# Performance work log

Measured on AMD Instinct MI355X. Metric: run time of the kernel, lower is better.

The kernel has to match this reference:

```python
import jax, jax.numpy as jnp
import numpy as np
import math

H = 16          # n_heads
D = 1024        # hidden_dim
HD = D // H     # head_dim = 64
LR = 256        # Linformer low-rank length L
MAX_T = 4096    # max_seq_len


def setup_inputs() -> dict:
    key = jax.random.key(0)
    ks = jax.random.split(key, 7)
    X = jax.random.normal(ks[0], (4, 4096, D), dtype=jnp.float32)
    # lecun_normal ~ N(0, 1/fan_in)
    W_kernel = jax.random.normal(ks[1], (D, 3 * D), dtype=jnp.float32) / math.sqrt(D)
    W_bias = jnp.zeros((3 * D,), dtype=jnp.float32)
    low_rank_E = jax.random.normal(ks[2], (MAX_T, H, LR), dtype=jnp.float32) / math.sqrt(MAX_T)
    low_rank_V = jax.random.normal(ks[3], (MAX_T, H, LR), dtype=jnp.float32) / math.sqrt(MAX_T)
    o_kernel = jax.random.normal(ks[4], (D, D), dtype=jnp.float32) / math.sqrt(D)
    o_bias = jnp.zeros((D,), dtype=jnp.float32)
    return {"X": X, "W_kernel": W_kernel, "W_bias": W_bias,
            "low_rank_E": low_rank_E, "low_rank_V": low_rank_V,
            "o_kernel": o_kernel, "o_bias": o_bias}


def reference(X, W_kernel, W_bias, low_rank_E, low_rank_V, o_kernel, o_bias):
    B, T, _ = X.shape
    # L2-normalize tokens
    norm = jnp.linalg.norm(X, ord=2, axis=-1, keepdims=True)  # (B,T,1)
    Xn = X / norm
    # fused QKV projection
    qkv = Xn @ W_kernel + W_bias                 # (B,T,3D)
    qkv = qkv.reshape(B, T, 3, H, HD)
    Q, K, V = qkv[:, :, 0], qkv[:, :, 1], qkv[:, :, 2]   # (B,T,H,HD)
    # low-rank sequence projection of K/V: T -> L
    E = low_rank_E[:T]                            # (T,H,L)
    F = low_rank_V[:T]                            # (T,H,L)
    Kp = jnp.einsum('THK,BTHD->BHKD', E, K)       # (B,H,L,HD)
    Vp = jnp.einsum('THK,BTHD->BHKD', F, V)       # (B,H,L,HD)
    Qh = Q.transpose(0, 2, 1, 3)                  # (B,H,T,HD)
    logits = jnp.einsum('BHTD,BHKD->BHTK', Qh, Kp) / math.sqrt(HD)
    attn = jax.nn.softmax(logits, axis=-1)        # (B,H,T,L)
    out = jnp.einsum('BHTK,BHKD->BHTD', attn, Vp) # (B,H,T,HD)
    out = out.transpose(0, 2, 1, 3).reshape(B, T, H * HD)
    return out @ o_kernel + o_bias
```

## Files before the change

### kernel.cpp

```cpp
#include <hip/hip_runtime.h>
#include <stdint.h>

typedef unsigned short u16;
typedef uint32_t u32;
typedef __bf16 bf16x8 __attribute__((ext_vector_type(8)));
typedef float f32x4 __attribute__((ext_vector_type(4)));

__device__ __forceinline__ u16 f2bf(float f) {
    u32 u = __builtin_bit_cast(u32, f);
    u += 0x7fffu + ((u >> 16) & 1u);
    return (u16)(u >> 16);
}

__device__ __forceinline__ f32x4 mfma16(bf16x8 a, bf16x8 b, f32x4 c) {
    return __builtin_amdgcn_mfma_f32_16x16x32_bf16(a, b, c, 0, 0, 0);
}

__device__ __forceinline__ void gld_lds16(void* lds, const void* g) {
    __builtin_amdgcn_global_load_lds(
        (__attribute__((address_space(1))) void*)(uintptr_t)g,
        (__attribute__((address_space(3))) void*)(u32)(uintptr_t)lds,
        16, 0, 0);
}

__global__ __launch_bounds__(256) void k_norm(const float* __restrict__ X,
                                              u16* __restrict__ Xn) {
    const int row = blockIdx.x;
    const float4 v = ((const float4*)(X + (size_t)row * 1024))[threadIdx.x];
    float ss = v.x * v.x + v.y * v.y + v.z * v.z + v.w * v.w;
#pragma unroll
    for (int m = 1; m < 64; m <<= 1) ss += __shfl_xor(ss, m);
    __shared__ float red[4];
    if ((threadIdx.x & 63) == 0) red[threadIdx.x >> 6] = ss;
    __syncthreads();
    const float sc = 1.0f / sqrtf(red[0] + red[1] + red[2] + red[3]);
    ushort4 o;
    o.x = f2bf(v.x * sc); o.y = f2bf(v.y * sc);
    o.z = f2bf(v.z * sc); o.w = f2bf(v.w * sc);
    ((ushort4*)(Xn + (size_t)row * 1024))[threadIdx.x] = o;
}

__global__ __launch_bounds__(256) void k_transpose_cast64(
    const float* __restrict__ src, u16* __restrict__ dst,
    int R, int rstride, long zsrc, long zdst) {
    __shared__ float tile[64][65];
    src += (size_t)blockIdx.z * zsrc;
    dst += (size_t)blockIdx.z * zdst;
    const int c0 = blockIdx.x * 64, r0 = blockIdx.y * 64;
    const int tid = threadIdx.x;
    const int lr = tid >> 4, lc = tid & 15;
#pragma unroll
    for (int i = 0; i < 4; ++i) {
        const int r = lr + i * 16;
        const float4 v = *(const float4*)(src + (size_t)(r0 + r) * rstride + c0 + lc * 4);
        tile[r][lc * 4 + 0] = v.x; tile[r][lc * 4 + 1] = v.y;
        tile[r][lc * 4 + 2] = v.z; tile[r][lc * 4 + 3] = v.w;
    }
    __syncthreads();
    const int c = tid >> 2, seg = tid & 3;
    u32 w[8];
#pragma unroll
    for (int j = 0; j < 8; ++j) {
        const u32 lo = f2bf(tile[seg * 16 + 2 * j][c]);
        const u32 hi = f2bf(tile[seg * 16 + 2 * j + 1][c]);
        w[j] = lo | (hi << 16);
    }
    u16* dp = dst + (size_t)(c0 + c) * R + r0 + seg * 16;
    uint4 q0; q0.x = w[0]; q0.y = w[1]; q0.z = w[2]; q0.w = w[3];
    uint4 q1; q1.x = w[4]; q1.y = w[5]; q1.z = w[6]; q1.w = w[7];
    *(uint4*)dp = q0;
    *((uint4*)dp + 1) = q1;
}

#define G256_PRE(Aptr, Bptr, LDA_, LDB_)                                          \
    const int tid = threadIdx.x, lane = tid & 63, wid = tid >> 6;                 \
    const int wm = wid >> 2, wn = wid & 3;                                        \
    const int cl = lane & 15, g = lane >> 4;                                      \
    const int srow = tid >> 2;                                                    \
    const int scol = ((tid & 3) ^ ((tid >> 3) & 3)) * 8;                          \
    const u16* pA0 = (Aptr) + (size_t)(m0 + srow) * (LDA_) + scol;                \
    const u16* pA1 = pA0 + (size_t)128 * (LDA_);                                  \
    const u16* pB0 = (Bptr) + (size_t)(n0 + srow) * (LDB_) + scol;                \
    const u16* pB1 = pB0 + (size_t)128 * (LDB_);                                  \
    u32 offA[8], offB[4];                                                         \
    _Pragma("unroll")                                                             \
    for (int mf = 0; mf < 8; ++mf) {                                              \
        const int r = wm * 128 + mf * 16 + cl;                                    \
        offA[mf] = r * 64 + ((g ^ ((r >> 1) & 3)) * 16);                          \
    }                                                                             \
    _Pragma("unroll")                                                             \
    for (int nf = 0; nf < 4; ++nf) {                                              \
        const int r = wn * 64 + nf * 16 + cl;                                     \
        offB[nf] = 65536 + r * 64 + ((g ^ ((r >> 1) & 3)) * 16);                  \
    }

#define G256_STAGE(kt)                                                            \
    {                                                                             \
        const u32 bo = ((kt) & 3) * 16384;                                        \
        gld_lds16(sm + bo + tid * 16,                 pA0 + (kt) * 32);           \
        gld_lds16(sm + bo + 8192 + tid * 16,          pA1 + (kt) * 32);           \
        gld_lds16(sm + 65536 + bo + tid * 16,         pB0 + (kt) * 32);           \
        gld_lds16(sm + 65536 + bo + 8192 + tid * 16,  pB1 + (kt) * 32);           \
    }

#define G256_LOOP(NKT)                                                            \
    G256_STAGE(0) G256_STAGE(1) G256_STAGE(2)                                     \
    for (int kt = 0; kt < (NKT); ++kt) {                                          \
        if (kt < (NKT) - 3) {                                                     \
            G256_STAGE(kt + 3)                                                    \
            asm volatile("s_waitcnt vmcnt(12)" ::: "memory");                     \
        } else if (kt == (NKT) - 3) {                                             \
            asm volatile("s_waitcnt vmcnt(8)" ::: "memory");                      \
        } else if (kt == (NKT) - 2) {                                             \
            asm volatile("s_waitcnt vmcnt(4)" ::: "memory");                      \
        } else {                                                                  \
            asm volatile("s_waitcnt vmcnt(0)" ::: "memory");                      \
        }                                                                         \
        __builtin_amdgcn_s_barrier();                                             \
        const char* bk = sm + (kt & 3) * 16384;                                   \
        bf16x8 aF[4], bF[4];                                                      \
        _Pragma("unroll")                                                         \
        for (int mf = 0; mf < 4; ++mf) aF[mf] = *(const bf16x8*)(bk + offA[mf]);  \
        _Pragma("unroll")                                                         \
        for (int nf = 0; nf < 4; ++nf) bF[nf] = *(const bf16x8*)(bk + offB[nf]);  \
        asm volatile("s_waitcnt lgkmcnt(0)" ::: "memory");                        \
        __builtin_amdgcn_sched_barrier(0);                                        \
        __builtin_amdgcn_s_setprio(1);                                            \
        _Pragma("unroll")                                                         \
        for (int mf = 0; mf < 4; ++mf)                                            \
            _Pragma("unroll")                                                     \
            for (int nf = 0; nf < 4; ++nf)                                        \
                acc[mf][nf] = mfma16(aF[mf], bF[nf], acc[mf][nf]);                \
        __builtin_amdgcn_s_setprio(0);                                            \
        bf16x8 aG[4];                                                             \
        _Pragma("unroll")                                                         \
        for (int mf = 0; mf < 4; ++mf) aG[mf] = *(const bf16x8*)(bk + offA[mf + 4]); \
        asm volatile("s_waitcnt lgkmcnt(0)" ::: "memory");                        \
        __builtin_amdgcn_sched_barrier(0);                                        \
        __builtin_amdgcn_s_setprio(1);                                            \
        _Pragma("unroll")                                                         \
        for (int mf = 0; mf < 4; ++mf)                                            \
            _Pragma("unroll")                                                     \
            for (int nf = 0; nf < 4; ++nf)                                        \
                acc[mf + 4][nf] = mfma16(aG[mf], bF[nf], acc[mf + 4][nf]);        \
        __builtin_amdgcn_s_setprio(0);                                            \
        __builtin_amdgcn_s_barrier();                                             \
    }

__global__ __launch_bounds__(512, 2) void k_gemm_qkv(
    const u16* __restrict__ A, const u16* __restrict__ Bt,
    const float* __restrict__ bias,
    u16* __restrict__ Qo, u16* __restrict__ Kt, u16* __restrict__ Vt) {
    __shared__ __align__(16) char sm[131072];
    u32 bid = blockIdx.x;
    bid = (bid & 7) * 96 + (bid >> 3);
    const int m0 = (int)(bid / 12) * 256, n0 = (int)(bid % 12) * 256;

    G256_PRE(A, Bt, 1024, 1024)

    const f32x4 fz = {0.f, 0.f, 0.f, 0.f};
    f32x4 acc[8][4];
#pragma unroll
    for (int i = 0; i < 8; ++i)
#pragma unroll
        for (int j = 0; j < 4; ++j) acc[i][j] = fz;

    G256_LOOP(32)

#pragma unroll
    for (int mf = 0; mf < 8; ++mf) {
        const int mbase = m0 + wm * 128 + mf * 16 + g * 4;
        const int b = mbase >> 12;
        const int t = mbase & 4095;
#pragma unroll
        for (int nf = 0; nf < 4; ++nf) {
            const int n = n0 + wn * 64 + nf * 16 + cl;
            const float bv = bias[n];
            const int seg = n >> 10;
            const int hd = n & 1023;
            f32x4 v = acc[mf][nf];
            if (seg == 0) {
#pragma unroll
                for (int r = 0; r < 4; ++r)
                    Qo[(size_t)(mbase + r) * 1024 + hd] = f2bf(v[r] + bv);
            } else {
                u16* dst = (seg == 1) ? Kt : Vt;
                ushort4 pk;
                pk.x = f2bf(v[0] + bv); pk.y = f2bf(v[1] + bv);
                pk.z = f2bf(v[2] + bv); pk.w = f2bf(v[3] + bv);
                *(ushort4*)(dst + (size_t)(b * 1024 + hd) * 4096 + t) = pk;
            }
        }
    }
}

__global__ __launch_bounds__(512, 2) void k_gemm_out(
    const u16* __restrict__ A, const u16* __restrict__ Bt,
    const float* __restrict__ bias, float* __restrict__ out) {
    __shared__ __align__(16) char sm[131072];
    u32 bid = blockIdx.x;
    bid = (bid & 7) * 32 + (bid >> 3);
    const int m0 = (int)(bid / 4) * 256, n0 = (int)(bid % 4) * 256;

    G256_PRE(A, Bt, 1024, 1024)

    const f32x4 fz = {0.f, 0.f, 0.f, 0.f};
    f32x4 acc[8][4];
#pragma unroll
    for (int i = 0; i < 8; ++i)
#pragma unroll
        for (int j = 0; j < 4; ++j) acc[i][j] = fz;

    G256_LOOP(32)

#pragma unroll
    for (int mf = 0; mf < 8; ++mf) {
        const int mbase = m0 + wm * 128 + mf * 16 + g * 4;
#pragma unroll
        for (int nf = 0; nf < 4; ++nf) {
            const int n = n0 + wn * 64 + nf * 16 + cl;
            const float bv = bias[n];
            f32x4 v = acc[mf][nf];
#pragma unroll
            for (int r = 0; r < 4; ++r)
                out[(size_t)(mbase + r) * 1024 + n] = v[r] + bv;
        }
    }
}

__global__ __launch_bounds__(256) void k_gemm_kpvp(
    const u16* __restrict__ Et, const u16* __restrict__ Ft,
    const u16* __restrict__ Kt, const u16* __restrict__ Vt,
    u16* __restrict__ Kp, u16* __restrict__ Vpt) {
    __shared__ __align__(16) char sm[24576];
    const int tid = threadIdx.x, lane = tid & 63, wid = tid >> 6;
    const int wm = wid >> 1, wn = wid & 1;
    const int cl = lane & 15, g = lane >> 4;
    const int mT = blockIdx.x;
    const int bh = blockIdx.y;
    const int h = bh & 15;
    const int s = blockIdx.z;

    const u16* Abase = (s == 0 ? Et : Ft) + (size_t)h * (256 * 4096);
    const u16* Bbase = (s == 0 ? Kt : Vt) + (size_t)bh * (64 * 4096);
    const u16* gA0 = Abase + (size_t)(mT * 128 + (tid >> 2)) * 4096 + (tid & 3) * 8;
    const u16* gA1 = gA0 + (size_t)64 * 4096;
    const u16* gB0 = Bbase + (size_t)(tid >> 2) * 4096 + (tid & 3) * 8;

    const f32x4 fz = {0.f, 0.f, 0.f, 0.f};
    f32x4 acc[4][2];
#pragma unroll
    for (int i = 0; i < 4; ++i) { acc[i][0] = fz; acc[i][1] = fz; }

    gld_lds16(sm + tid * 16, gA0); gld_lds16(sm + 4096 + tid * 16, gA1);
    gld_lds16(sm + 8192 + tid * 16, gB0);
    gA0 += 32; gA1 += 32; gB0 += 32;

    u32 roff = 0;
    for (int k0 = 0; k0 < 4096; k0 += 32) {
        const u32 woff = roff ^ 12288;
        if (k0 + 32 < 4096) {
            gld_lds16(sm + woff + tid * 16, gA0); gld_lds16(sm + woff + 4096 + tid * 16, gA1);
            gld_lds16(sm + woff + 8192 + tid * 16, gB0);
            gA0 += 32; gA1 += 32; gB0 += 32;
            asm volatile("s_waitcnt vmcnt(3)" ::: "memory");
        } else {
            asm volatile("s_waitcnt vmcnt(0)" ::: "memory");
        }
        __builtin_amdgcn_s_barrier();
        __builtin_amdgcn_sched_barrier(0);
        const char* rb = sm + roff;
        bf16x8 aF[4], bF[2];
#pragma unroll
        for (int mf = 0; mf < 4; ++mf)
            aF[mf] = *(const bf16x8*)(rb + (wm * 64 + mf * 16 + cl) * 64 + g * 16);
#pragma unroll
        for (int nf = 0; nf < 2; ++nf)
            bF[nf] = *(const bf16x8*)(rb + 8192 + (wn * 32 + nf * 16 + cl) * 64 + g * 16);
#pragma unroll
        for (int mf = 0; mf < 4; ++mf)
#pragma unroll
            for (int nf = 0; nf < 2; ++nf)
                acc[mf][nf] = mfma16(aF[mf], bF[nf], acc[mf][nf]);
        asm volatile("s_waitcnt lgkmcnt(0)" ::: "memory");
        __builtin_amdgcn_s_barrier();
        roff = woff;
    }

    const size_t obase = (size_t)bh * 16384;
#pragma unroll
    for (int mf = 0; mf < 4; ++mf) {
        const int m = mT * 128 + wm * 64 + mf * 16 + g * 4;
#pragma unroll
        for (int nf = 0; nf < 2; ++nf) {
            const int n = wn * 32 + nf * 16 + cl;
            f32x4 v = acc[mf][nf];
            if (s == 0) {
#pragma unroll
                for (int r = 0; r < 4; ++r)
                    Kp[obase + (size_t)(m + r) * 64 + n] = f2bf(v[r]);
            } else {
                ushort4 pk;
                pk.x = f2bf(v[0]); pk.y = f2bf(v[1]);
                pk.z = f2bf(v[2]); pk.w = f2bf(v[3]);
                *(ushort4*)(Vpt + obase + (size_t)n * 256 + m) = pk;
            }
        }
    }
}

__global__ __launch_bounds__(256, 1) void k_attn(
    const u16* __restrict__ Q, const u16* __restrict__ Kp,
    const u16* __restrict__ Vpt, u16* __restrict__ AO) {
    __shared__ __align__(16) char sm[65536];
    const int lane = threadIdx.x & 63, wid = threadIdx.x >> 6;
    const int cl = lane & 15, g = lane >> 4;
    const int tT = blockIdx.x, h = blockIdx.y, b = blockIdx.z;
    const int bh = b * 16 + h;
    const int trow0 = b * 4096 + tT * 128 + wid * 32;
    const u16* Qb = Q + (size_t)trow0 * 1024 + h * 64;
    const u16* KpB = Kp + (size_t)bh * (256 * 64);
    const u16* VpB = Vpt + (size_t)bh * (64 * 256);
    char* sP = sm + wid * 16384;

    bf16x8 qF[2][2];
#pragma unroll
    for (int nf = 0; nf < 2; ++nf)
#pragma unroll
        for (int ks = 0; ks < 2; ++ks)
            qF[nf][ks] = *(const bf16x8*)(Qb + (size_t)(nf * 16 + cl) * 1024 + ks * 32 + g * 8);

    const f32x4 fz = {0.f, 0.f, 0.f, 0.f};
    f32x4 Sp[16][2];
#pragma unroll
    for (int mf = 0; mf < 16; ++mf) { Sp[mf][0] = fz; Sp[mf][1] = fz; }

#pragma unroll
    for (int mf = 0; mf < 16; ++mf) {
#pragma unroll
        for (int ks = 0; ks < 2; ++ks) {
            bf16x8 aF = *(const bf16x8*)(KpB + (size_t)(mf * 16 + cl) * 64 + ks * 32 + g * 8);
            Sp[mf][0] = mfma16(aF, qF[0][ks], Sp[mf][0]);
            Sp[mf][1] = mfma16(aF, qF[1][ks], Sp[mf][1]);
        }
    }

    float inv_sum[2];
#pragma unroll
    for (int nf = 0; nf < 2; ++nf) {
        float mx = -1e30f;
#pragma unroll
        for (int mf = 0; mf < 16; ++mf)
#pragma unroll
            for (int r = 0; r < 4; ++r) {
                float x = Sp[mf][nf][r] * 0.125f;
                Sp[mf][nf][r] = x;
                mx = fmaxf(mx, x);
            }
        mx = fmaxf(mx, __shfl_xor(mx, 16));
        mx = fmaxf(mx, __shfl_xor(mx, 32));
        float sum = 0.f;
#pragma unroll
        for (int mf = 0; mf < 16; ++mf)
#pragma unroll
            for (int r = 0; r < 4; ++r) {
                float p = __expf(Sp[mf][nf][r] - mx);
                Sp[mf][nf][r] = p;
                sum += p;
            }
        sum += __shfl_xor(sum, 16);
        sum += __shfl_xor(sum, 32);
        inv_sum[nf] = 1.0f / sum;

        const int tl = nf * 16 + cl;
        const int sw = (tl & 7) << 4;
#pragma unroll
        for (int mf = 0; mf < 16; ++mf) {
            uint2 pk;
            pk.x = (u32)f2bf(Sp[mf][nf][0]) | ((u32)f2bf(Sp[mf][nf][1]) << 16);
            pk.y = (u32)f2bf(Sp[mf][nf][2]) | ((u32)f2bf(Sp[mf][nf][3]) << 16);
            *(uint2*)(sP + ((tl * 512 + (mf * 16 + g * 4) * 2) ^ sw)) = pk;
        }
    }

    f32x4 Oa[4][2];
#pragma unroll
    for (int mf = 0; mf < 4; ++mf) { Oa[mf][0] = fz; Oa[mf][1] = fz; }
#pragma unroll
    for (int ks = 0; ks < 8; ++ks) {
        bf16x8 aF[4];
#pragma unroll
        for (int mf = 0; mf < 4; ++mf)
            aF[mf] = *(const bf16x8*)(VpB + (size_t)(mf * 16 + cl) * 256 + ks * 32 + g * 8);
#pragma unroll
        for (int nf = 0; nf < 2; ++nf) {
            const int tl = nf * 16 + cl;
            const int sw = (tl & 7) << 4;
            bf16x8 bF = *(const bf16x8*)(sP + ((tl * 512 + (ks * 32 + g * 8) * 2) ^ sw));
#pragma unroll
            for (int mf = 0; mf < 4; ++mf)
                Oa[mf][nf] = mfma16(aF[mf], bF, Oa[mf][nf]);
        }
    }

#pragma unroll
    for (int nf = 0; nf < 2; ++nf) {
        const int t = trow0 + nf * 16 + cl;
#pragma unroll
        for (int mf = 0; mf < 4; ++mf) {
            f32x4 v = Oa[mf][nf];
            ushort4 pk;
            pk.x = f2bf(v[0] * inv_sum[nf]); pk.y = f2bf(v[1] * inv_sum[nf]);
            pk.z = f2bf(v[2] * inv_sum[nf]); pk.w = f2bf(v[3] * inv_sum[nf]);
            *(ushort4*)(AO + (size_t)t * 1024 + h * 64 + mf * 16 + g * 4) = pk;
        }
    }
}

extern "C" void kernel_launch(void* const* d_in, const int* in_sizes, int n_in,
                              void* d_out, int out_size, void* d_ws, size_t ws_size,
                              hipStream_t stream) {
    const float* X  = (const float*)d_in[0];
    const float* Wk = (const float*)d_in[1];
    const float* Wb = (const float*)d_in[2];
    const float* E  = (const float*)d_in[3];
    const float* F  = (const float*)d_in[4];
    const float* Ok = (const float*)d_in[5];
    const float* Ob = (const float*)d_in[6];
    float* out = (float*)d_out;
    char* ws = (char*)d_ws;

    u16* Xn  = (u16*)(ws + 0);
    u16* Wt  = (u16*)(ws + 33554432);
    u16* Ot  = (u16*)(ws + 39845888);
    u16* Et  = (u16*)(ws + 41943040);
    u16* Ft  = (u16*)(ws + 75497472);
    u16* Qb  = (u16*)(ws + 109051904);
    u16* Kt  = (u16*)(ws + 142606336);
    u16* Vt  = (u16*)(ws + 176160768);
    u16* Kp  = (u16*)(ws + 209715200);
    u16* Vpt = (u16*)(ws + 211812352);
    u16* AO  = Xn;

    k_norm<<<16384, 256, 0, stream>>>(X, Xn);
    k_transpose_cast64<<<dim3(48, 16, 1), 256, 0, stream>>>(Wk, Wt, 1024, 3072, 0, 0);
    k_transpose_cast64<<<dim3(16, 16, 1), 256, 0, stream>>>(Ok, Ot, 1024, 1024, 0, 0);
    k_transpose_cast64<<<dim3(4, 64, 16), 256, 0, stream>>>(E, Et, 4096, 4096, 256, 1048576);
    k_transpose_cast64<<<dim3(4, 64, 16), 256, 0, stream>>>(F, Ft, 4096, 4096, 256, 1048576);
    k_gemm_qkv<<<768, 512, 0, stream>>>(Xn, Wt, Wb, Qb, Kt, Vt);
    k_gemm_kpvp<<<dim3(2, 64, 2), 256, 0, stream>>>(Et, Ft, Kt, Vt, Kp, Vpt);
    k_attn<<<dim3(32, 16, 4), 256, 0, stream>>>(Qb, Kp, Vpt, AO);
    k_gemm_out<<<256, 512, 0, stream>>>(AO, Ot, Ob, out);
}
```

Baseline: 404.5 us.

## Rework 256x256 GEMM main loop to K=64 double-buffered stages with interleaved loads

Replaces the 4-stage K=32 pipeline in the QKV and output projection GEMMs with a 2-buffer K=64 scheme. Each LDS stage is split into four quarter-tiles, and global-to-LDS loads for the next stage are issued between MFMA groups to overlap copy with compute. It also changes the LDS swizzle to a 128-byte row XOR pattern and halves the number of barrier-synchronised iterations. The tradeoff is more barriers per stage, since one follows each quarter MMA block, and reduced prefetch depth.

After: 387.7 us. 1.04x faster.

```diff
diff --git a/kernel.cpp b/kernel.cpp
--- a/kernel.cpp
+++ b/kernel.cpp
@@ -72,79 +72,94 @@
     *((uint4*)dp + 1) = q1;
 }
 
-#define G256_PRE(Aptr, Bptr, LDA_, LDB_)                                          \
-    const int tid = threadIdx.x, lane = tid & 63, wid = tid >> 6;                 \
-    const int wm = wid >> 2, wn = wid & 3;                                        \
-    const int cl = lane & 15, g = lane >> 4;                                      \
-    const int srow = tid >> 2;                                                    \
-    const int scol = ((tid & 3) ^ ((tid >> 3) & 3)) * 8;                          \
-    const u16* pA0 = (Aptr) + (size_t)(m0 + srow) * (LDA_) + scol;                \
-    const u16* pA1 = pA0 + (size_t)128 * (LDA_);                                  \
-    const u16* pB0 = (Bptr) + (size_t)(n0 + srow) * (LDB_) + scol;                \
-    const u16* pB1 = pB0 + (size_t)128 * (LDB_);                                  \
-    u32 offA[8], offB[4];                                                         \
-    _Pragma("unroll")                                                             \
-    for (int mf = 0; mf < 8; ++mf) {                                              \
-        const int r = wm * 128 + mf * 16 + cl;                                    \
-        offA[mf] = r * 64 + ((g ^ ((r >> 1) & 3)) * 16);                          \
-    }                                                                             \
-    _Pragma("unroll")                                                             \
-    for (int nf = 0; nf < 4; ++nf) {                                              \
-        const int r = wn * 64 + nf * 16 + cl;                                     \
-        offB[nf] = 65536 + r * 64 + ((g ^ ((r >> 1) & 3)) * 16);                  \
-    }
-
-#define G256_STAGE(kt)                                                            \
-    {                                                                             \
-        const u32 bo = ((kt) & 3) * 16384;                                        \
-        gld_lds16(sm + bo + tid * 16,                 pA0 + (kt) * 32);           \
-        gld_lds16(sm + bo + 8192 + tid * 16,          pA1 + (kt) * 32);           \
-        gld_lds16(sm + 65536 + bo + tid * 16,         pB0 + (kt) * 32);           \
-        gld_lds16(sm + 65536 + bo + 8192 + tid * 16,  pB1 + (kt) * 32);           \
-    }
-
-#define G256_LOOP(NKT)                                                            \
-    G256_STAGE(0) G256_STAGE(1) G256_STAGE(2)                                     \
-    for (int kt = 0; kt < (NKT); ++kt) {                                          \
-        if (kt < (NKT) - 3) {                                                     \
-            G256_STAGE(kt + 3)                                                    \
-            asm volatile("s_waitcnt vmcnt(12)" ::: "memory");                     \
-        } else if (kt == (NKT) - 3) {                                             \
-            asm volatile("s_waitcnt vmcnt(8)" ::: "memory");                      \
-        } else if (kt == (NKT) - 2) {                                             \
-            asm volatile("s_waitcnt vmcnt(4)" ::: "memory");                      \
-        } else {                                                                  \
-            asm volatile("s_waitcnt vmcnt(0)" ::: "memory");                      \
-        }                                                                         \
-        __builtin_amdgcn_s_barrier();                                             \
-        const char* bk = sm + (kt & 3) * 16384;                                   \
-        bf16x8 aF[4], bF[4];                                                      \
-        _Pragma("unroll")                                                         \
-        for (int mf = 0; mf < 4; ++mf) aF[mf] = *(const bf16x8*)(bk + offA[mf]);  \
-        _Pragma("unroll")                                                         \
-        for (int nf = 0; nf < 4; ++nf) bF[nf] = *(const bf16x8*)(bk + offB[nf]);  \
-        asm volatile("s_waitcnt lgkmcnt(0)" ::: "memory");                        \
-        __builtin_amdgcn_sched_barrier(0);                                        \
-        __builtin_amdgcn_s_setprio(1);                                            \
-        _Pragma("unroll")                                                         \
-        for (int mf = 0; mf < 4; ++mf)                                            \
-            _Pragma("unroll")                                                     \
-            for (int nf = 0; nf < 4; ++nf)                                        \
-                acc[mf][nf] = mfma16(aF[mf], bF[nf], acc[mf][nf]);                \
-        __builtin_amdgcn_s_setprio(0);                                            \
-        bf16x8 aG[4];                                                             \
-        _Pragma("unroll")                                                         \
-        for (int mf = 0; mf < 4; ++mf) aG[mf] = *(const bf16x8*)(bk + offA[mf + 4]); \
-        asm volatile("s_waitcnt lgkmcnt(0)" ::: "memory");                        \
-        __builtin_amdgcn_sched_barrier(0);                                        \
-        __builtin_amdgcn_s_setprio(1);                                            \
-        _Pragma("unroll")                                                         \
-        for (int mf = 0; mf < 4; ++mf)                                            \
-            _Pragma("unroll")                                                     \
-            for (int nf = 0; nf < 4; ++nf)                                        \
-                acc[mf + 4][nf] = mfma16(aG[mf], bF[nf], acc[mf + 4][nf]);        \
-        __builtin_amdgcn_s_setprio(0);                                            \
-        __builtin_amdgcn_s_barrier();                                             \
+#define G8_PRE(Aptr, Bptr)                                                       \
+    const int tid = threadIdx.x, lane = tid & 63;                                \
+    const int wid = tid >> 6, wm = wid >> 2, wn = wid & 3;                       \
+    const int cl = lane & 15, g = lane >> 4;                                     \
+    const int colb = (tid & 7) * 16;                                             \
+    const int scb = colb ^ (((tid >> 3) & 7) << 4);                              \
+    const int rbA = ((tid >> 3) & 31) + ((tid >> 8) << 7);                       \
+    const int rbB = tid >> 3;                                                    \
+    const char* gA = (const char*)(Aptr) + (size_t)(m0 + rbA) * 2048 + scb;      \
+    const char* gB = (const char*)(Bptr) + (size_t)(n0 + rbB) * 2048 + scb;      \
+    const u32 lA = (u32)(rbA * 128 + colb);                                      \
+    const u32 lB = (u32)(65536 + rbB * 128 + colb);                              \
+    const int xr0 = (g * 16) ^ ((cl & 7) << 4);                                  \
+    const int xr1 = (64 + g * 16) ^ ((cl & 7) << 4);
+
+#define G8_STA(q, tau, beta) gld_lds16(sm + (beta) + lA + (q) * 4096,            \
+                                       gA + (q) * 65536 + (size_t)(tau) * 128);
+#define G8_STB(c, tau, beta) gld_lds16(sm + (beta) + lB + (c) * 8192,            \
+                                       gB + (c) * 131072 + (size_t)(tau) * 128);
+
+#define G8_RDB(beta)                                                             \
+    _Pragma("unroll") for (int nf = 0; nf < 4; ++nf) {                           \
+        const u32 rb_ = (beta) + 65536 + (u32)(wn * 64 + nf * 16 + cl) * 128;    \
+        bF[nf][0] = *(const bf16x8*)(sm + rb_ + xr0);                            \
+        bF[nf][1] = *(const bf16x8*)(sm + rb_ + xr1);                            \
+    }
+#define G8_RDA(q, beta)                                                          \
+    _Pragma("unroll") for (int m = 0; m < 2; ++m) {                              \
+        const u32 ra_ = (beta) + (u32)(wm * 128 + (q) * 32 + m * 16 + cl) * 128; \
+        aF[m][0] = *(const bf16x8*)(sm + ra_ + xr0);                             \
+        aF[m][1] = *(const bf16x8*)(sm + ra_ + xr1);                             \
+    }
+
+#define G8_MMA(q)                                                                \
+    asm volatile("s_waitcnt lgkmcnt(0)" ::: "memory");                           \
+    __builtin_amdgcn_sched_barrier(0);                                           \
+    __builtin_amdgcn_s_setprio(1);                                               \
+    _Pragma("unroll") for (int m = 0; m < 2; ++m)                                \
+        _Pragma("unroll") for (int nf = 0; nf < 4; ++nf) {                       \
+            acc[(q)*2 + m][nf] = mfma16(aF[m][0], bF[nf][0], acc[(q)*2 + m][nf]);\
+            acc[(q)*2 + m][nf] = mfma16(aF[m][1], bF[nf][1], acc[(q)*2 + m][nf]);\
+        }                                                                        \
+    __builtin_amdgcn_s_setprio(0);                                               \
+    __builtin_amdgcn_s_barrier();                                                \
+    __builtin_amdgcn_sched_barrier(0);
+
+#define G8_LOOP                                                                  \
+    bf16x8 aF[2][2], bF[4][2];                                                   \
+    G8_STA(0, 0, 0) G8_STB(0, 0, 0) G8_STA(1, 0, 0) G8_STB(1, 0, 0)              \
+    G8_STA(2, 0, 0) G8_STB(2, 0, 0) G8_STA(3, 0, 0) G8_STB(3, 0, 0)              \
+    G8_STA(0, 1, 32768) G8_STB(0, 1, 32768)                                      \
+    G8_STA(1, 1, 32768) G8_STB(1, 1, 32768)                                      \
+    G8_STA(2, 1, 32768) G8_STB(2, 1, 32768)                                      \
+    for (int it = 0; it < 8; ++it) {                                             \
+        const int t1 = 2 * it + 1, t2v = 2 * it + 2, t3v = 2 * it + 3;           \
+        const bool nt = (it < 7);                                                \
+                                                                         \
+        G8_STA(3, t1, 32768) G8_STB(3, t1, 32768)                                \
+        asm volatile("s_waitcnt vmcnt(8)" ::: "memory");                         \
+        __builtin_amdgcn_s_barrier();                                            \
+        G8_RDB(0) G8_RDA(0, 0) G8_MMA(0)                                         \
+                                                                         \
+        if (nt) { G8_STA(0, t2v, 0) G8_STB(0, t2v, 0) }                          \
+        G8_RDA(1, 0) G8_MMA(1)                                                   \
+                                                                         \
+        if (nt) { G8_STA(1, t2v, 0) G8_STB(1, t2v, 0) }                          \
+        G8_RDA(2, 0) G8_MMA(2)                                                   \
+                                                                         \
+        if (nt) { G8_STA(2, t2v, 0) G8_STB(2, t2v, 0) }                          \
+        G8_RDA(3, 0) G8_MMA(3)                                                   \
+                                                                         \
+        if (nt) {                                                                \
+            G8_STA(3, t2v, 0) G8_STB(3, t2v, 0)                                  \
+            asm volatile("s_waitcnt vmcnt(8)" ::: "memory");                     \
+        } else {                                                                 \
+            asm volatile("s_waitcnt vmcnt(0)" ::: "memory");                     \
+        }                                                                        \
+        __builtin_amdgcn_s_barrier();                                            \
+        G8_RDB(32768) G8_RDA(0, 32768) G8_MMA(0)                                 \
+                                                                         \
+        if (nt) { G8_STA(0, t3v, 32768) G8_STB(0, t3v, 32768) }                  \
+        G8_RDA(1, 32768) G8_MMA(1)                                               \
+                                                                         \
+        if (nt) { G8_STA(1, t3v, 32768) G8_STB(1, t3v, 32768) }                  \
+        G8_RDA(2, 32768) G8_MMA(2)                                               \
+                                                                         \
+        if (nt) { G8_STA(2, t3v, 32768) G8_STB(2, t3v, 32768) }                  \
+        G8_RDA(3, 32768) G8_MMA(3)                                               \
     }
 
 __global__ __launch_bounds__(512, 2) void k_gemm_qkv(
@@ -156,7 +171,7 @@
     bid = (bid & 7) * 96 + (bid >> 3);
     const int m0 = (int)(bid / 12) * 256, n0 = (int)(bid % 12) * 256;
 
-    G256_PRE(A, Bt, 1024, 1024)
+    G8_PRE(A, Bt)
 
     const f32x4 fz = {0.f, 0.f, 0.f, 0.f};
     f32x4 acc[8][4];
@@ -165,7 +180,7 @@
 #pragma unroll
         for (int j = 0; j < 4; ++j) acc[i][j] = fz;
 
-    G256_LOOP(32)
+    G8_LOOP
 
 #pragma unroll
     for (int mf = 0; mf < 8; ++mf) {
@@ -202,7 +217,7 @@
     bid = (bid & 7) * 32 + (bid >> 3);
     const int m0 = (int)(bid / 4) * 256, n0 = (int)(bid % 4) * 256;
 
-    G256_PRE(A, Bt, 1024, 1024)
+    G8_PRE(A, Bt)
 
     const f32x4 fz = {0.f, 0.f, 0.f, 0.f};
     f32x4 acc[8][4];
@@ -211,7 +226,7 @@
 #pragma unroll
         for (int j = 0; j < 4; ++j) acc[i][j] = fz;
 
-    G256_LOOP(32)
+    G8_LOOP
 
 #pragma unroll
     for (int mf = 0; mf < 8; ++mf) {
```
